# Kernel tuning notes

Measured on AMD Instinct MI355X. Metric: run time of the kernel, lower is better.

Reference implementation:

```python
import jax, jax.numpy as jnp
import numpy as np

B, S, H = 32, 256, 128
K, C, DSUB, O = 8, 4096, 16, 6  # PQ subspaces, ncentroids=4096, subvector dim, bits/symbol


def setup_inputs() -> dict:
    key = jax.random.key(0)
    ks = jax.random.split(key, 8)
    return {
        "z": jax.random.normal(ks[0], (B, S, 3), jnp.float32),
        "W1": jax.random.normal(ks[1], (3, H), jnp.float32) * 0.3,
        "b1": jax.random.normal(ks[2], (H,), jnp.float32) * 0.1,
        "W2": jax.random.normal(ks[3], (H, H), jnp.float32) * 0.1,
        "b2": jax.random.normal(ks[4], (H,), jnp.float32) * 0.1,
        "centroids": jax.random.normal(ks[5], (K, C, DSUB), jnp.float32),
        "W3": jax.random.normal(ks[6], (H, O), jnp.float32) * 0.1,
        "b3": jax.random.normal(ks[7], (O,), jnp.float32) * 0.1,
    }


def reference(z, W1, b1, W2, b2, centroids, W3, b3):
    # Small demapper MLP (layers 1-2, exact dense math)
    h1 = jax.nn.relu(z @ W1 + b1)            # [B,S,H]
    h2 = jax.nn.relu(h1 @ W2 + b2)           # [B,S,H] == layer3in
    N = B * S
    x = h2.reshape(N, K, DSUB)               # split rows into K PQ subvectors
    # Encode: nearest centroid per subspace (||x-c||^2 argmin; ||x||^2 is constant per row)
    dots = jnp.einsum("nkd,kcd->nkc", x, centroids)      # [N,K,C]
    c_norm = jnp.sum(centroids * centroids, axis=-1)      # [K,C]
    codes = jnp.argmin(c_norm[None, :, :] - 2.0 * dots, axis=-1)  # [N,K] int
    # LUT: precomputed centroid @ W3 per subspace
    W3r = W3.reshape(K, DSUB, O)
    lut = jnp.einsum("kcd,kdo->kco", centroids, W3r)      # [K,C,O]
    # Approximate matmul: sum of LUT entries selected by codes
    approx = jnp.sum(lut[jnp.arange(K)[None, :], codes], axis=1)  # [N,O]
    llr = (approx + b3).reshape(B, S * O)                 # [B, n]
    return llr
```

## Files before the change

kernel.cpp:

```cpp
#include <hip/hip_runtime.h>
#include <hip/hip_fp16.h>
#include <stdint.h>

#define NROWS 8192
#define HDIM  128
#define KSUB  8
#define NC    4096
#define DSUB  16
#define OUTD  6

#define FB_TAU 6e-5f
#define DOTSCALE (-2.0f / 4096.0f)

typedef _Float16 f16x8 __attribute__((ext_vector_type(8)));
typedef float    f32x4 __attribute__((ext_vector_type(4)));

#define XK_OFF 0u
#define CN_OFF 4194304u
#define B1_OFF 4325376u
#define PK_OFF 6422528u

__global__ __launch_bounds__(256) void prep_kernel(
    const float* __restrict__ z, const float* __restrict__ W1, const float* __restrict__ b1,
    const float* __restrict__ W2, const float* __restrict__ b2,
    const float* __restrict__ ce,
    float* __restrict__ xk, float* __restrict__ cnorm, f16x8* __restrict__ B1S)
{
    __shared__ float h1s[16 * HDIM];
    __shared__ float w2s[HDIM * HDIM];
    const int t = threadIdx.x;
    const int row0 = blockIdx.x * 16;

    {
        const int e = blockIdx.x * 256 + t;
        const int k    = e >> 14;
        const int tile = (e >> 6) & 255;
        const int lane = e & 63;
        const int col  = lane & 15;
        const int quad = lane >> 4;
        const int dims = (quad & 1) * 8;
        const int part = quad >> 1;
        const int n = tile * 16 + col;
        const float* cp = &ce[((size_t)k * NC + n) * DSUB + dims];
        f16x8 hi, lo;
        #pragma unroll
        for (int j = 0; j < 8; ++j) {
            const float s = cp[j] * 16.0f;
            const _Float16 h = (_Float16)s;
            hi[j] = h;
            lo[j] = (_Float16)(s - (float)h);
        }
        B1S[e] = part ? lo : hi;
    }

    if (blockIdx.x < (KSUB * NC) / 256) {
        const int g = blockIdx.x * 256 + t;
        const float4* cp = (const float4*)&ce[(size_t)g * DSUB];
        float nn = 0.f;
        #pragma unroll
        for (int q = 0; q < 4; ++q) {
            const float4 v = cp[q];
            nn = fmaf(v.x, v.x, nn); nn = fmaf(v.y, v.y, nn);
            nn = fmaf(v.z, v.z, nn); nn = fmaf(v.w, v.w, nn);
        }
        cnorm[g] = nn;
    }

    {
        const float4* g4 = (const float4*)W2;
        float4* s4 = (float4*)w2s;
        #pragma unroll
        for (int q = 0; q < 16; ++q) s4[t + q * 256] = g4[t + q * 256];
    }

    #pragma unroll
    for (int e = 0; e < 8; ++e) {
        const int idx = e * 256 + t;
        const int r = idx >> 7, j = idx & 127;
        const int n = row0 + r;
        float acc = b1[j];
        acc = fmaf(z[n * 3 + 0], W1[0 * HDIM + j], acc);
        acc = fmaf(z[n * 3 + 1], W1[1 * HDIM + j], acc);
        acc = fmaf(z[n * 3 + 2], W1[2 * HDIM + j], acc);
        h1s[idx] = fmaxf(acc, 0.f);
    }
    __syncthreads();

    const int c4 = (t & 31) * 4;
    const int r2 = (t >> 5) * 2;
    float acc[2][4];
    #pragma unroll
    for (int a = 0; a < 2; ++a)
        #pragma unroll
        for (int b = 0; b < 4; ++b) acc[a][b] = 0.f;

    for (int k4 = 0; k4 < HDIM; k4 += 4) {
        float hh[2][4], ww[4][4];
        #pragma unroll
        for (int q = 0; q < 2; ++q) {
            const float4 v = *(const float4*)&h1s[(r2 + q) * HDIM + k4];
            hh[q][0] = v.x; hh[q][1] = v.y; hh[q][2] = v.z; hh[q][3] = v.w;
        }
        #pragma unroll
        for (int p = 0; p < 4; ++p) {
            const float4 v = *(const float4*)&w2s[(k4 + p) * HDIM + c4];
            ww[p][0] = v.x; ww[p][1] = v.y; ww[p][2] = v.z; ww[p][3] = v.w;
        }
        #pragma unroll
        for (int q = 0; q < 2; ++q)
            #pragma unroll
            for (int p = 0; p < 4; ++p) {
                acc[q][0] = fmaf(hh[q][p], ww[p][0], acc[q][0]);
                acc[q][1] = fmaf(hh[q][p], ww[p][1], acc[q][1]);
                acc[q][2] = fmaf(hh[q][p], ww[p][2], acc[q][2]);
                acc[q][3] = fmaf(hh[q][p], ww[p][3], acc[q][3]);
            }
    }

    const float4 bb = *(const float4*)&b2[c4];
    const int kk = c4 >> 4;
    const int dd = c4 & 15;
    #pragma unroll
    for (int q = 0; q < 2; ++q) {
        float4 o;
        o.x = fmaxf(acc[q][0] + bb.x, 0.f);
        o.y = fmaxf(acc[q][1] + bb.y, 0.f);
        o.z = fmaxf(acc[q][2] + bb.z, 0.f);
        o.w = fmaxf(acc[q][3] + bb.w, 0.f);
        *(float4*)&xk[((size_t)kk * NROWS + (row0 + r2 + q)) * DSUB + dd] = o;
    }
}

__global__ __launch_bounds__(256, 4) void argmin_kernel(
    const float* __restrict__ xk, const f16x8* __restrict__ B1S,
    const float* __restrict__ cnorm, unsigned* __restrict__ pk)
{
    __shared__ f16x8 cs[8 * 64];
    __shared__ float cnL[NC];
    const int t = threadIdx.x;
    const int lane = t & 63;
    const int wid  = t >> 6;
    const int k  = blockIdx.y;
    const int rb = blockIdx.x * 4 + wid;
    const int col  = lane & 15;
    const int quad = lane >> 4;
    const int dims = (quad & 1) * 8;
    const int part = quad >> 1;

    {
        const float* cnp0 = &cnorm[k * NC];
        #pragma unroll
        for (int q = 0; q < 16; ++q) cnL[t + q * 256] = cnp0[t + q * 256];
    }

    f16x8 A[4];
    #pragma unroll
    for (int g = 0; g < 4; ++g) {
        const int row = rb * 64 + g * 16 + col;
        const float* xp = &xk[((size_t)k * NROWS + row) * DSUB + dims];
        f16x8 hi, lo;
        #pragma unroll
        for (int j = 0; j < 8; ++j) {
            const float s = xp[j] * 256.0f;
            const _Float16 h = (_Float16)s;
            hi[j] = h;
            lo[j] = (_Float16)(s - (float)h);
        }
        A[g] = part ? lo : hi;
    }

    float m1[4][4], m2[4][4];
    int   idx[4][4];
    #pragma unroll
    for (int g = 0; g < 4; ++g)
        #pragma unroll
        for (int j = 0; j < 4; ++j) { m1[g][j] = 1e30f; m2[g][j] = 1e30f; idx[g][j] = 0; }

    const f16x8* gp = &B1S[(size_t)k * 256 * 64];

    uint4 pre0, pre1;
    {
        const uint4* g4 = (const uint4*)gp;
        pre0 = g4[t];
        pre1 = g4[t + 256];
    }

    for (int ch = 0; ch < 32; ++ch) {
        __syncthreads();
        {
            uint4* s4 = (uint4*)cs;
            s4[t] = pre0;
            s4[t + 256] = pre1;
        }
        __syncthreads();
        if (ch < 31) {
            const uint4* g4 = (const uint4*)(gp + (size_t)(ch + 1) * 512);
            pre0 = g4[t];
            pre1 = g4[t + 256];
        }

        #pragma unroll 2
        for (int tt = 0; tt < 8; ++tt) {
            const f16x8 b1 = cs[tt * 64 + lane];
            const f16x8 b2 = cs[tt * 64 + (lane ^ 32)];
            const float nrm = cnL[(ch * 8 + tt) * 16 + col];
            const f32x4 zz = {0.f, 0.f, 0.f, 0.f};
            const int c = ((ch * 8 + tt) << 4) + col;
            #pragma unroll
            for (int g = 0; g < 4; ++g) {
                f32x4 p = __builtin_amdgcn_mfma_f32_16x16x32_f16(A[g], b1, zz, 0, 0, 0);
                p       = __builtin_amdgcn_mfma_f32_16x16x32_f16(A[g], b2, p, 0, 0, 0);
                #pragma unroll
                for (int j = 0; j < 4; ++j) {
                    const float s = fmaf(p[j], DOTSCALE, nrm);
                    const bool lt = s < m1[g][j];
                    m2[g][j] = __builtin_amdgcn_fmed3f(s, m1[g][j], m2[g][j]);
                    idx[g][j] = lt ? c : idx[g][j];
                    m1[g][j] = fminf(s, m1[g][j]);
                }
            }
        }
    }

    #pragma unroll
    for (int off = 1; off < 16; off <<= 1) {
        #pragma unroll
        for (int g = 0; g < 4; ++g)
            #pragma unroll
            for (int j = 0; j < 4; ++j) {
                const float om1 = __shfl_xor(m1[g][j], off, 64);
                const float om2 = __shfl_xor(m2[g][j], off, 64);
                const int  oidx = __shfl_xor(idx[g][j], off, 64);
                const bool better = (om1 < m1[g][j]) ||
                                    (om1 == m1[g][j] && oidx < idx[g][j]);
                m2[g][j] = fminf(fminf(m2[g][j], om2), fmaxf(m1[g][j], om1));
                m1[g][j] = better ? om1 : m1[g][j];
                idx[g][j] = better ? oidx : idx[g][j];
            }
    }

    if (col == 0) {
        #pragma unroll
        for (int g = 0; g < 4; ++g)
            #pragma unroll
            for (int j = 0; j < 4; ++j) {
                const int row = rb * 64 + g * 16 + quad * 4 + j;
                const unsigned short dh =
                    __half_as_ushort(__float2half(m2[g][j] - m1[g][j]));
                pk[(size_t)row * KSUB + k] =
                    ((unsigned)dh << 16) | (unsigned)idx[g][j];
            }
    }
}

__global__ __launch_bounds__(256) void finish_kernel(
    const float* __restrict__ xk, const float* __restrict__ ce,
    const float* __restrict__ cnorm, const unsigned* __restrict__ pk,
    const float* __restrict__ W3, const float* __restrict__ b3,
    float* __restrict__ out)
{
    __shared__ int codes_s[256];
    __shared__ int wl_s[256];
    __shared__ int wcnt;
    const int t = threadIdx.x;
    const int row0 = blockIdx.x * 32;
    if (t == 0) wcnt = 0;
    __syncthreads();

    {
        const int row = row0 + (t >> 3);
        const int k = t & 7;
        const unsigned w = pk[(size_t)row * KSUB + k];
        codes_s[t] = (int)(w & 0xFFFFu);
        const float gap = (float)__ushort_as_half((unsigned short)(w >> 16));
        if (gap < FB_TAU) {
            const int slot = atomicAdd(&wcnt, 1);
            wl_s[slot] = t;
        }
    }
    __syncthreads();

    {
        const int lane = t & 63;
        const int wid = t >> 6;
        const int nitems = wcnt;
        for (int i = wid; i < nitems; i += 4) {
            const int wg = wl_s[i];
            const int row = row0 + (wg >> 3), k = wg & 7;
            float xr[DSUB];
            {
                const float* xp = &xk[((size_t)k * NROWS + row) * DSUB];
                #pragma unroll
                for (int q = 0; q < DSUB; q += 4) {
                    const float4 v = *(const float4*)&xp[q];
                    xr[q + 0] = -2.f * v.x; xr[q + 1] = -2.f * v.y;
                    xr[q + 2] = -2.f * v.z; xr[q + 3] = -2.f * v.w;
                }
            }
            float bm = 1e30f; int bi = NC;
            for (int c = lane; c < NC; c += 64) {
                const float* cp = &ce[((size_t)k * NC + c) * DSUB];
                float s = cnorm[k * NC + c];
                #pragma unroll
                for (int d = 0; d < DSUB; ++d) s = fmaf(xr[d], cp[d], s);
                if (s < bm) { bm = s; bi = c; }
            }
            #pragma unroll
            for (int off = 1; off < 64; off <<= 1) {
                const float om = __shfl_xor(bm, off, 64);
                const int  oi = __shfl_xor(bi, off, 64);
                const bool better = (om < bm) || (om == bm && oi < bi);
                bm = better ? om : bm;
                bi = better ? oi : bi;
            }
            if (lane == 0) codes_s[wg] = bi;
        }
    }
    __syncthreads();

    if (t < 32 * OUTD) {
        const int nl = t / OUTD;
        const int o = t - nl * OUTD;
        const int n = row0 + nl;
        float acc = b3[o];
        #pragma unroll
        for (int k = 0; k < KSUB; ++k) {
            const int code = codes_s[nl * KSUB + k];
            const float* cp = &ce[((size_t)k * NC + code) * DSUB];
            const float* wp = &W3[(k * DSUB) * OUTD + o];
            #pragma unroll
            for (int d = 0; d < DSUB; ++d)
                acc = fmaf(cp[d], wp[d * OUTD], acc);
        }
        out[n * OUTD + o] = acc;
    }
}

extern "C" void kernel_launch(void* const* d_in, const int* in_sizes, int n_in,
                              void* d_out, int out_size, void* d_ws, size_t ws_size,
                              hipStream_t stream)
{
    const float* z  = (const float*)d_in[0];
    const float* W1 = (const float*)d_in[1];
    const float* b1 = (const float*)d_in[2];
    const float* W2 = (const float*)d_in[3];
    const float* b2 = (const float*)d_in[4];
    const float* ce = (const float*)d_in[5];
    const float* W3 = (const float*)d_in[6];
    const float* b3 = (const float*)d_in[7];

    char* ws = (char*)d_ws;
    float* xk    = (float*)(ws + XK_OFF);
    float* cnorm = (float*)(ws + CN_OFF);
    f16x8* B1S   = (f16x8*)(ws + B1_OFF);
    unsigned* pk = (unsigned*)(ws + PK_OFF);

    hipLaunchKernelGGL(prep_kernel, dim3(512), dim3(256), 0, stream,
                       z, W1, b1, W2, b2, ce, xk, cnorm, B1S);
    hipLaunchKernelGGL(argmin_kernel, dim3(32, 8), dim3(256), 0, stream,
                       xk, B1S, cnorm, pk);
    hipLaunchKernelGGL(finish_kernel, dim3(256), dim3(256), 0, stream,
                       xk, ce, cnorm, pk, W3, b3, (float*)d_out);
}
```

Baseline: 184.5 us.

## Split argmin centroid range across four blocks and merge partial minima in finish

The argmin kernel grid gains a third dimension that splits the 4096 centroids into four 1024-wide chunks, so 1024 blocks run instead of 256 and fill the GPU better. Each block writes a 64-bit packed record (order-preserving min distance, gap, index). The finish kernel then merges the four partial results with a 64-bit min and rebuilds the second-best gap for the fallback test. This costs more pk traffic, four times the A-operand setup and an extra merge step.

```diff
diff --git a/kernel.cpp b/kernel.cpp
--- a/kernel.cpp
+++ b/kernel.cpp
@@ -133,14 +133,15 @@
 
 __global__ __launch_bounds__(256, 4) void argmin_kernel(
     const float* __restrict__ xk, const f16x8* __restrict__ B1S,
-    const float* __restrict__ cnorm, unsigned* __restrict__ pk)
+    const float* __restrict__ cnorm, unsigned long long* __restrict__ pk)
 {
     __shared__ f16x8 cs[8 * 64];
-    __shared__ float cnL[NC];
+    __shared__ float cnL[1024];
     const int t = threadIdx.x;
     const int lane = t & 63;
     const int wid  = t >> 6;
     const int k  = blockIdx.y;
+    const int cz = blockIdx.z;
     const int rb = blockIdx.x * 4 + wid;
     const int col  = lane & 15;
     const int quad = lane >> 4;
@@ -148,9 +149,9 @@
     const int part = quad >> 1;
 
     {
-        const float* cnp0 = &cnorm[k * NC];
-        #pragma unroll
-        for (int q = 0; q < 16; ++q) cnL[t + q * 256] = cnp0[t + q * 256];
+        const float* cnp0 = &cnorm[k * NC + cz * 1024];
+        #pragma unroll
+        for (int q = 0; q < 4; ++q) cnL[t + q * 256] = cnp0[t + q * 256];
     }
 
     f16x8 A[4];
@@ -176,7 +177,7 @@
         #pragma unroll
         for (int j = 0; j < 4; ++j) { m1[g][j] = 1e30f; m2[g][j] = 1e30f; idx[g][j] = 0; }
 
-    const f16x8* gp = &B1S[(size_t)k * 256 * 64];
+    const f16x8* gp = &B1S[((size_t)k * 256 + cz * 64) * 64];
 
     uint4 pre0, pre1;
     {
@@ -185,7 +186,7 @@
         pre1 = g4[t + 256];
     }
 
-    for (int ch = 0; ch < 32; ++ch) {
+    for (int ch = 0; ch < 8; ++ch) {
         __syncthreads();
         {
             uint4* s4 = (uint4*)cs;
@@ -193,7 +194,7 @@
             s4[t + 256] = pre1;
         }
         __syncthreads();
-        if (ch < 31) {
+        if (ch < 7) {
             const uint4* g4 = (const uint4*)(gp + (size_t)(ch + 1) * 512);
             pre0 = g4[t];
             pre1 = g4[t + 256];
@@ -205,7 +206,7 @@
             const f16x8 b2 = cs[tt * 64 + (lane ^ 32)];
             const float nrm = cnL[(ch * 8 + tt) * 16 + col];
             const f32x4 zz = {0.f, 0.f, 0.f, 0.f};
-            const int c = ((ch * 8 + tt) << 4) + col;
+            const int c = ((cz * 64 + ch * 8 + tt) << 4) + col;
             #pragma unroll
             for (int g = 0; g < 4; ++g) {
                 f32x4 p = __builtin_amdgcn_mfma_f32_16x16x32_f16(A[g], b1, zz, 0, 0, 0);
@@ -245,9 +246,12 @@
             #pragma unroll
             for (int j = 0; j < 4; ++j) {
                 const int row = rb * 64 + g * 16 + quad * 4 + j;
+                unsigned u = __float_as_uint(m1[g][j]);
+                u = (u & 0x80000000u) ? ~u : (u | 0x80000000u);
                 const unsigned short dh =
                     __half_as_ushort(__float2half(m2[g][j] - m1[g][j]));
-                pk[(size_t)row * KSUB + k] =
+                pk[((size_t)cz * NROWS + row) * KSUB + k] =
+                    ((unsigned long long)u << 32) |
                     ((unsigned)dh << 16) | (unsigned)idx[g][j];
             }
     }
@@ -255,7 +259,7 @@
 
 __global__ __launch_bounds__(256) void finish_kernel(
     const float* __restrict__ xk, const float* __restrict__ ce,
-    const float* __restrict__ cnorm, const unsigned* __restrict__ pk,
+    const float* __restrict__ cnorm, const unsigned long long* __restrict__ pk,
     const float* __restrict__ W3, const float* __restrict__ b3,
     float* __restrict__ out)
 {
@@ -270,10 +274,26 @@
     {
         const int row = row0 + (t >> 3);
         const int k = t & 7;
-        const unsigned w = pk[(size_t)row * KSUB + k];
-        codes_s[t] = (int)(w & 0xFFFFu);
-        const float gap = (float)__ushort_as_half((unsigned short)(w >> 16));
-        if (gap < FB_TAU) {
+        unsigned long long p[4];
+        #pragma unroll
+        for (int s = 0; s < 4; ++s)
+            p[s] = pk[((size_t)s * NROWS + row) * KSUB + k];
+        unsigned long long w = p[0];
+        #pragma unroll
+        for (int s = 1; s < 4; ++s) w = p[s] < w ? p[s] : w;
+        const unsigned uw = (unsigned)(w >> 32);
+        const float m1w = __uint_as_float((uw & 0x80000000u) ? (uw ^ 0x80000000u) : ~uw);
+        float m2g = m1w + (float)__ushort_as_half((unsigned short)((unsigned)w >> 16));
+        #pragma unroll
+        for (int s = 0; s < 4; ++s) {
+            if (p[s] != w) {
+                const unsigned us = (unsigned)(p[s] >> 32);
+                m2g = fminf(m2g, __uint_as_float(
+                    (us & 0x80000000u) ? (us ^ 0x80000000u) : ~us));
+            }
+        }
+        codes_s[t] = (int)(w & 0xFFFFull);
+        if (m2g - m1w < FB_TAU) {
             const int slot = atomicAdd(&wcnt, 1);
             wl_s[slot] = t;
         }
@@ -353,11 +373,11 @@
     float* xk    = (float*)(ws + XK_OFF);
     float* cnorm = (float*)(ws + CN_OFF);
     f16x8* B1S   = (f16x8*)(ws + B1_OFF);
-    unsigned* pk = (unsigned*)(ws + PK_OFF);
+    unsigned long long* pk = (unsigned long long*)(ws + PK_OFF);
 
     hipLaunchKernelGGL(prep_kernel, dim3(512), dim3(256), 0, stream,
                        z, W1, b1, W2, b2, ce, xk, cnorm, B1S);
-    hipLaunchKernelGGL(argmin_kernel, dim3(32, 8), dim3(256), 0, stream,
+    hipLaunchKernelGGL(argmin_kernel, dim3(32, 8, 4), dim3(256), 0, stream,
                        xk, B1S, cnorm, pk);
     hipLaunchKernelGGL(finish_kernel, dim3(256), dim3(256), 0, stream,
                        xk, ce, cnorm, pk, W3, b3, (float*)d_out);
```

Result: faster. 176.6 us (-4.3%).
